# Optimization experiments

Measured on AMD Instinct MI355X. Metric: run time of the kernel, lower is better.

The kernel has to match this reference:

```python
import jax, jax.numpy as jnp
import numpy as np


def setup_inputs() -> dict:
    key = jax.random.key(0)
    k1, k2, k3 = jax.random.split(key, 3)
    B, Na, Nb = 64, 8192, 8192
    phases_a = jax.random.normal(k1, (B, Na), dtype=jnp.float32)
    phases_b = jax.random.normal(k2, (B, Nb), dtype=jnp.float32)
    # Binary coupled-pair indicator mask (N_a, N_b)
    coupling_mask = jax.random.randint(k3, (Na, Nb), 0, 2, dtype=jnp.int32)
    return {"phases_a": phases_a, "phases_b": phases_b, "coupling_mask": coupling_mask}


def reference(phases_a, phases_b, coupling_mask):
    """Masked phase-locking value (PLV) between two oscillator banks.

    Mathematically identical to |sum_ij M_ij * exp(i*(a_i - b_j))| / sum(M),
    but computed via trig identities + matmul instead of materializing the
    O(B*Na*Nb) complex tensor:
      real = sum_ij M_ij (cos a_i cos b_j + sin a_i sin b_j)
      imag = sum_ij M_ij (sin a_i cos b_j - cos a_i sin b_j)
    """
    ca, sa = jnp.cos(phases_a), jnp.sin(phases_a)   # (B, Na)
    cb, sb = jnp.cos(phases_b), jnp.sin(phases_b)   # (B, Nb)
    M = coupling_mask.astype(ca.dtype)              # (Na, Nb)
    caM = ca @ M                                    # (B, Nb)
    saM = sa @ M                                    # (B, Nb)
    real = jnp.sum(caM * cb + saM * sb, axis=-1)    # (B,)
    imag = jnp.sum(saM * cb - caM * sb, axis=-1)    # (B,)
    n_pairs = jnp.maximum(M.sum(), jnp.asarray(1.0, ca.dtype))
    return jnp.sqrt(real * real + imag * imag) / n_pairs
```

## Files before the change

### kernel.cpp

```cpp
#include <hip/hip_runtime.h>
#include <hip/hip_bf16.h>

#define NA 8192
#define NB 8192
#define NBATCH 64
#define NC 128
#define BM 128
#define WM 32
#define SPLITK 8
#define KCHUNK (NB / SPLITK)

#define XT_BYTES  (NC * NB * 2)
#define CTR_OFF   XT_BYTES
#define PPART_OFF (CTR_OFF + 4096)

typedef __bf16 bf16x8 __attribute__((ext_vector_type(8)));
typedef float  f32x4  __attribute__((ext_vector_type(4)));

__global__ __launch_bounds__(256) void prep_b_kernel(
    const float* __restrict__ pb, __hip_bfloat16* __restrict__ Xtf)
{
    int tid = blockIdx.x * 256 + threadIdx.x;
    int b = tid >> 13;
    int k = tid & (NB - 1);

    float ph = pb[tid];
    float s, c;
    __sincosf(ph, &s, &c);

    int kstep = k >> 5;
    int quad  = (k >> 3) & 3;
    int e     = k & 7;
    int t     = b >> 3;
    int m0    = (2 * b) & 15;
    size_t base = ((size_t)(kstep * 8 + t) * 64 + quad * 16) * 8 + e;
    Xtf[base + (size_t)m0 * 8]       = __float2bfloat16(c);
    Xtf[base + (size_t)(m0 + 1) * 8] = __float2bfloat16(s);
}

__global__ __launch_bounds__(256, 2) void gemm_kernel(
    const int* __restrict__ mask, const __hip_bfloat16* __restrict__ Xtfg,
    float* __restrict__ Ppart, int* __restrict__ count)
{
    const int tid  = threadIdx.x;
    const int wave = tid >> 6;
    const int lane = tid & 63;
    const int quad = lane >> 4;
    const int m    = lane & 15;
    const int itile = blockIdx.x;
    const int kc    = blockIdx.y;
    const int k0    = kc * KCHUNK;

    const int rowbase = itile * BM + wave * WM;
    const bf16x8* __restrict__ xf = reinterpret_cast<const bf16x8*>(Xtfg);

    f32x4 acc[2][8];
#pragma unroll
    for (int f = 0; f < 2; ++f)
#pragma unroll
        for (int t = 0; t < 8; ++t)
            acc[f][t] = (f32x4){0.f, 0.f, 0.f, 0.f};

    int cnt = 0;

    for (int kk = k0; kk < k0 + KCHUNK; kk += 32) {
        const int kq = kk + quad * 8;

        bf16x8 a[2];
#pragma unroll
        for (int f = 0; f < 2; ++f) {
            const int4* p = reinterpret_cast<const int4*>(
                mask + (size_t)(rowbase + f * 16 + m) * NB + kq);
            int4 r0 = p[0];
            int4 r1 = p[1];
            cnt += r0.x + r0.y + r0.z + r0.w + r1.x + r1.y + r1.z + r1.w;
            uint4 u;
            u.x = (r0.x ? 0x3F80u : 0u) | (r0.y ? 0x3F800000u : 0u);
            u.y = (r0.z ? 0x3F80u : 0u) | (r0.w ? 0x3F800000u : 0u);
            u.z = (r1.x ? 0x3F80u : 0u) | (r1.y ? 0x3F800000u : 0u);
            u.w = (r1.z ? 0x3F80u : 0u) | (r1.w ? 0x3F800000u : 0u);
            a[f] = __builtin_bit_cast(bf16x8, u);
        }

        const bf16x8* fx = xf + (size_t)(kk >> 5) * 8 * 64 + lane;
#pragma unroll
        for (int t = 0; t < 8; ++t) {
            const bf16x8 bfrag = fx[t * 64];
            acc[0][t] = __builtin_amdgcn_mfma_f32_16x16x32_bf16(a[0], bfrag, acc[0][t], 0, 0, 0);
            acc[1][t] = __builtin_amdgcn_mfma_f32_16x16x32_bf16(a[1], bfrag, acc[1][t], 0, 0, 0);
        }
    }

    float* pout = Ppart + (size_t)kc * NA * NC;
#pragma unroll
    for (int f = 0; f < 2; ++f)
#pragma unroll
        for (int t = 0; t < 8; ++t)
#pragma unroll
            for (int r = 0; r < 4; ++r) {
                int row = rowbase + f * 16 + quad * 4 + r;
                int col = t * 16 + m;
                pout[(size_t)row * NC + col] = acc[f][t][r];
            }

#pragma unroll
    for (int off = 32; off > 0; off >>= 1) cnt += __shfl_down(cnt, off);
    if (lane == 0) atomicAdd(count, cnt);
}

__global__ __launch_bounds__(256) void reduce_kernel(
    const float* __restrict__ pa, const float* __restrict__ Ppart,
    float* __restrict__ realg, float* __restrict__ imagg)
{
    const int t = threadIdx.x;
    const int c = t & 127;
    const int half = t >> 7;
    const int b = c >> 1;
    const int odd = c & 1;
    const int i0 = blockIdx.x * 32;

    float pacc = 0.f, qacc = 0.f;
    for (int i = i0 + half; i < i0 + 32; i += 2) {
        float v = 0.f;
#pragma unroll
        for (int kc = 0; kc < SPLITK; ++kc)
            v += Ppart[(size_t)kc * NA * NC + (size_t)i * NC + c];
        float ph = pa[(size_t)b * NA + i];
        float sn, cs;
        __sincosf(ph, &sn, &cs);
        float yc = odd ? sn : cs;
        float yo = odd ? cs : sn;
        pacc += yc * v;
        qacc += odd ? -(yo * v) : (yo * v);
    }

    __shared__ float red[2][256];
    red[0][t] = pacc;
    red[1][t] = qacc;
    __syncthreads();
    if (t < 128) {
        red[0][t] = red[0][t] + red[0][t + 128];
        red[1][t] = red[1][t] + red[1][t + 128];
    }
    __syncthreads();
    if (t < 64) {
        float real = red[0][2 * t] + red[0][2 * t + 1];
        float imag = red[1][2 * t] + red[1][2 * t + 1];
        atomicAdd(&realg[t], real);
        atomicAdd(&imagg[t], imag);
    }
}

__global__ void finalize_kernel(const float* __restrict__ realg,
                                const float* __restrict__ imagg,
                                const int* __restrict__ count,
                                float* __restrict__ out)
{
    int t = threadIdx.x;
    if (t < NBATCH) {
        float r = realg[t], im = imagg[t];
        float n = fmaxf((float)(*count), 1.0f);
        out[t] = sqrtf(r * r + im * im) / n;
    }
}

extern "C" void kernel_launch(void* const* d_in, const int* in_sizes, int n_in,
                              void* d_out, int out_size, void* d_ws, size_t ws_size,
                              hipStream_t stream) {
    const float* pa   = (const float*)d_in[0];
    const float* pb   = (const float*)d_in[1];
    const int*   mask = (const int*)d_in[2];
    float* out = (float*)d_out;

    char* ws = (char*)d_ws;
    __hip_bfloat16* Xtf = (__hip_bfloat16*)ws;
    float* realg = (float*)(ws + CTR_OFF);
    float* imagg = realg + 64;
    int*   count = (int*)(ws + CTR_OFF + 512);
    float* Ppart = (float*)(ws + PPART_OFF);

    hipMemsetAsync(ws + CTR_OFF, 0, 4096, stream);

    prep_b_kernel<<<(NBATCH * NB) / 256, 256, 0, stream>>>(pb, Xtf);

    dim3 g(NA / BM, SPLITK);
    gemm_kernel<<<g, 256, 0, stream>>>(mask, Xtf, Ppart, count);

    reduce_kernel<<<NA / 32, 256, 0, stream>>>(pa, Ppart, realg, imagg);

    finalize_kernel<<<1, 64, 0, stream>>>(realg, imagg, count, out);
}
```

Baseline: 433.4 us.

## Fuse phase-a trig reduction into GEMM epilogue and drop split-K partial buffer

The GEMM epilogue now computes sin/cos of phases_a and reduces each accumulator tile directly to per-batch real/imag partials per block, using shuffles and shared memory. This replaces writing and re-reading a large split-K partial matrix and a separate reduce kernel. A single-block final kernel sums the per-block partials deterministically. Mask loads also become nontemporal so the streamed mask does not pollute the cache. In exchange the epilogue does more trig work and gathers pa with strided loads, which adds pressure on the GEMM kernel's tail.

```diff
diff --git a/kernel.cpp b/kernel.cpp
--- a/kernel.cpp
+++ b/kernel.cpp
@@ -9,13 +9,15 @@
 #define WM 32
 #define SPLITK 8
 #define KCHUNK (NB / SPLITK)
+#define NBLK (SPLITK * NA / BM)
 
-#define XT_BYTES  (NC * NB * 2)
-#define CTR_OFF   XT_BYTES
-#define PPART_OFF (CTR_OFF + 4096)
+#define XT_BYTES (NC * NB * 2)
+#define CTR_OFF  XT_BYTES
+#define PBLK_OFF (CTR_OFF + 512)
 
 typedef __bf16 bf16x8 __attribute__((ext_vector_type(8)));
 typedef float  f32x4  __attribute__((ext_vector_type(4)));
+typedef int    ivec4  __attribute__((ext_vector_type(4)));
 
 __global__ __launch_bounds__(256) void prep_b_kernel(
     const float* __restrict__ pb, __hip_bfloat16* __restrict__ Xtf)
@@ -40,7 +42,8 @@
 
 __global__ __launch_bounds__(256, 2) void gemm_kernel(
     const int* __restrict__ mask, const __hip_bfloat16* __restrict__ Xtfg,
-    float* __restrict__ Ppart, int* __restrict__ count)
+    const float* __restrict__ pa,
+    float* __restrict__ Pblk, int* __restrict__ count)
 {
     const int tid  = threadIdx.x;
     const int wave = tid >> 6;
@@ -69,10 +72,10 @@
         bf16x8 a[2];
 #pragma unroll
         for (int f = 0; f < 2; ++f) {
-            const int4* p = reinterpret_cast<const int4*>(
+            const ivec4* p = reinterpret_cast<const ivec4*>(
                 mask + (size_t)(rowbase + f * 16 + m) * NB + kq);
-            int4 r0 = p[0];
-            int4 r1 = p[1];
+            ivec4 r0 = __builtin_nontemporal_load(p);
+            ivec4 r1 = __builtin_nontemporal_load(p + 1);
             cnt += r0.x + r0.y + r0.z + r0.w + r1.x + r1.y + r1.z + r1.w;
             uint4 u;
             u.x = (r0.x ? 0x3F80u : 0u) | (r0.y ? 0x3F800000u : 0u);
@@ -91,74 +94,69 @@
         }
     }
 
-    float* pout = Ppart + (size_t)kc * NA * NC;
+    __shared__ float lred[4][64][2];
+    const int odd = m & 1;
+
 #pragma unroll
-    for (int f = 0; f < 2; ++f)
+    for (int t = 0; t < 8; ++t) {
+        const int b = t * 8 + (m >> 1);
+        float rc = 0.f, ic = 0.f;
 #pragma unroll
-        for (int t = 0; t < 8; ++t)
+        for (int f = 0; f < 2; ++f)
 #pragma unroll
             for (int r = 0; r < 4; ++r) {
                 int row = rowbase + f * 16 + quad * 4 + r;
-                int col = t * 16 + m;
-                pout[(size_t)row * NC + col] = acc[f][t][r];
+                float ph = pa[(size_t)b * NA + row];
+                float sn, cs;
+                __sincosf(ph, &sn, &cs);
+                float Ax = odd ? sn : cs;
+                float Bx = odd ? -cs : sn;
+                rc = fmaf(Ax, acc[f][t][r], rc);
+                ic = fmaf(Bx, acc[f][t][r], ic);
             }
+        rc += __shfl_xor(rc, 1);  ic += __shfl_xor(ic, 1);
+        rc += __shfl_xor(rc, 16); ic += __shfl_xor(ic, 16);
+        rc += __shfl_xor(rc, 32); ic += __shfl_xor(ic, 32);
+        if (quad == 0 && !odd) {
+            lred[wave][b][0] = rc;
+            lred[wave][b][1] = ic;
+        }
+    }
+    __syncthreads();
+
+    if (tid < 128) {
+        float s = lred[0][tid >> 1][tid & 1] + lred[1][tid >> 1][tid & 1]
+                + lred[2][tid >> 1][tid & 1] + lred[3][tid >> 1][tid & 1];
+        int bid = blockIdx.y * 64 + blockIdx.x;
+        Pblk[(size_t)bid * 128 + tid] = s;
+    }
 
 #pragma unroll
     for (int off = 32; off > 0; off >>= 1) cnt += __shfl_down(cnt, off);
     if (lane == 0) atomicAdd(count, cnt);
 }
 
-__global__ __launch_bounds__(256) void reduce_kernel(
-    const float* __restrict__ pa, const float* __restrict__ Ppart,
-    float* __restrict__ realg, float* __restrict__ imagg)
+__global__ __launch_bounds__(512) void final_kernel(
+    const float* __restrict__ Pblk, const int* __restrict__ count,
+    float* __restrict__ out)
 {
     const int t = threadIdx.x;
-    const int c = t & 127;
-    const int half = t >> 7;
-    const int b = c >> 1;
-    const int odd = c & 1;
-    const int i0 = blockIdx.x * 32;
+    const int grp = t & 3;
+    const int idx = t >> 2;
 
-    float pacc = 0.f, qacc = 0.f;
-    for (int i = i0 + half; i < i0 + 32; i += 2) {
-        float v = 0.f;
-#pragma unroll
-        for (int kc = 0; kc < SPLITK; ++kc)
-            v += Ppart[(size_t)kc * NA * NC + (size_t)i * NC + c];
-        float ph = pa[(size_t)b * NA + i];
-        float sn, cs;
-        __sincosf(ph, &sn, &cs);
-        float yc = odd ? sn : cs;
-        float yo = odd ? cs : sn;
-        pacc += yc * v;
-        qacc += odd ? -(yo * v) : (yo * v);
-    }
+    float s = 0.f;
+#pragma unroll 8
+    for (int blk = grp * (NBLK / 4); blk < (grp + 1) * (NBLK / 4); ++blk)
+        s += Pblk[(size_t)blk * 128 + idx];
+    s += __shfl_xor(s, 1);
+    s += __shfl_xor(s, 2);
 
-    __shared__ float red[2][256];
-    red[0][t] = pacc;
-    red[1][t] = qacc;
+    __shared__ float red[128];
+    if (grp == 0) red[idx] = s;
     __syncthreads();
-    if (t < 128) {
-        red[0][t] = red[0][t] + red[0][t + 128];
-        red[1][t] = red[1][t] + red[1][t + 128];
-    }
-    __syncthreads();
-    if (t < 64) {
-        float real = red[0][2 * t] + red[0][2 * t + 1];
-        float imag = red[1][2 * t] + red[1][2 * t + 1];
-        atomicAdd(&realg[t], real);
-        atomicAdd(&imagg[t], imag);
-    }
-}
 
-__global__ void finalize_kernel(const float* __restrict__ realg,
-                                const float* __restrict__ imagg,
-                                const int* __restrict__ count,
-                                float* __restrict__ out)
-{
-    int t = threadIdx.x;
     if (t < NBATCH) {
-        float r = realg[t], im = imagg[t];
+        float r = red[2 * t], im = red[2 * t + 1];
         float n = fmaxf((float)(*count), 1.0f);
         out[t] = sqrtf(r * r + im * im) / n;
     }
@@ -174,19 +172,15 @@
 
     char* ws = (char*)d_ws;
     __hip_bfloat16* Xtf = (__hip_bfloat16*)ws;
-    float* realg = (float*)(ws + CTR_OFF);
-    float* imagg = realg + 64;
-    int*   count = (int*)(ws + CTR_OFF + 512);
-    float* Ppart = (float*)(ws + PPART_OFF);
+    int*   count = (int*)(ws + CTR_OFF);
+    float* Pblk  = (float*)(ws + PBLK_OFF);
 
-    hipMemsetAsync(ws + CTR_OFF, 0, 4096, stream);
+    hipMemsetAsync(ws + CTR_OFF, 0, 512, stream);
 
     prep_b_kernel<<<(NBATCH * NB) / 256, 256, 0, stream>>>(pb, Xtf);
 
     dim3 g(NA / BM, SPLITK);
-    gemm_kernel<<<g, 256, 0, stream>>>(mask, Xtf, Ppart, count);
+    gemm_kernel<<<g, 256, 0, stream>>>(mask, Xtf, pa, Pblk, count);
 
-    reduce_kernel<<<NA / 32, 256, 0, stream>>>(pa, Ppart, realg, imagg);
-
-    finalize_kernel<<<1, 64, 0, stream>>>(realg, imagg, count, out);
+    final_kernel<<<1, 512, 0, stream>>>(Pblk, count, out);
 }
```

Measured after the change: 419.7 us. 1.03x faster.
